# Performance work log

Measured on AMD Instinct MI355X. Metric: run time of the kernel, lower is better.

## Reference

```python
import jax, jax.numpy as jnp
import numpy as np

DT = 0.01
V_REST = 0.0


def setup_inputs() -> dict:
    key = jax.random.key(0)
    ks = jax.random.split(key, 9)
    S, N, T = 64, 128, 1000
    w = jax.random.normal(ks[0], (N, N), dtype=jnp.float32) / jnp.sqrt(jnp.float32(N))
    ic = jax.random.uniform(ks[1], (N,), dtype=jnp.float32)
    v0 = jax.random.uniform(ks[2], (S, N), dtype=jnp.float32)
    i0 = jax.random.uniform(ks[3], (S, N), dtype=jnp.float32)
    # spike-clock state starts at minus an Exponential(1) draw; event fires when it hits 0
    u0 = jax.random.uniform(ks[4], (S, N), dtype=jnp.float32, minval=1e-6, maxval=1.0)
    s0 = jnp.log(u0)
    mu = jax.random.uniform(ks[5], (2,), dtype=jnp.float32, minval=0.5, maxval=1.0)
    sg = jax.random.normal(ks[6], (2, 2), dtype=jnp.float32)
    sigma = 0.1 * jnp.dot(sg, sg.T)  # PSD diffusion matrix as in __init__
    noise = jax.random.normal(ks[7], (T, S, N, 2), dtype=jnp.float32)
    ue = jax.random.uniform(ks[8], (T, S, N), dtype=jnp.float32, minval=1e-6, maxval=1.0)
    exp_draws = -jnp.log(ue)
    return {"w": w, "ic": ic, "v0": v0, "i0": i0, "s0": s0,
            "mu": mu, "sigma": sigma, "noise": noise, "exp_draws": exp_draws}


def reference(w, ic, v0, i0, s0, mu, sigma, noise, exp_draws):
    """Euler-Maruyama integration of the spiking-neuron jump-SDE.

    Per neuron state y = (v, i, s):
      dv = mu1*(i + ic - v) dt + (sigma dW)_0
      di = -mu2*i dt        + (sigma dW)_1
      ds = intensity_fn(v) dt   (intensity_fn = softplus)
    Spike event when s crosses 0 (cond_fn = y[:, 2]):
      v -> v_rest, postsynaptic currents i += spikes @ w, s -> -Exp(1) redraw.
    Returns ys of shape (samples, neurons, times, 3).
    """
    mu1, mu2 = mu[0], mu[1]
    dW = noise * jnp.sqrt(jnp.asarray(DT, noise.dtype))  # [T,S,N,2]

    def step(carry, xs):
        v, i, s = carry
        dw, edraw = xs
        # drift
        dv = mu1 * (i + ic - v)
        di = -mu2 * i
        ds = jax.nn.softplus(v)  # intensity_fn
        # diffusion on (v,i) channels: sigma @ dW per neuron
        nvi = jnp.einsum('snk,jk->snj', dw, sigma)  # [S,N,2]
        v = v + DT * dv + nvi[..., 0]
        i = i + DT * di + nvi[..., 1]
        s = s + DT * ds
        spike = s >= 0.0  # event detection (cond_fn hits zero)
        spk = spike.astype(v.dtype)
        i = i + spk @ w                    # network coupling jump
        v = jnp.where(spike, V_REST, v)    # membrane reset
        s = jnp.where(spike, -edraw, s)    # redraw exponential spike clock
        return (v, i, s), jnp.stack([v, i, s], axis=-1)  # [S,N,3]

    (_, _, _), ys = jax.lax.scan(step, (v0, i0, s0), (dW, exp_draws))
    # ys: [T,S,N,3] -> [S,N,T,3] (samples, neurons, times, 3)
    return jnp.transpose(ys, (1, 2, 0, 3))
```

## Files before the change

kernel.cpp:

```cpp
#include <hip/hip_runtime.h>
#include <cmath>

#define NS 64
#define NN 128
#define NT 1000
#define CH 8
#define NNP 129
#define WROWS 130
#define WL_DW (WROWS * NN)
#define OB_HALF (CH * 3 * NNP)
#define OBUF_DW (2 * OB_HALF)
#define LDS_BYTES ((WL_DW + OBUF_DW) * 4 + 32)

__device__ __forceinline__ float softplus_np(float x) {
    float r = fmaxf(x, 0.0f) + log1pf(expf(-fabsf(x)));
    return (x == 0.0f) ? 0.693147180559945309f : r;
}

__device__ __forceinline__ void sync_lds() {
    __builtin_amdgcn_sched_barrier(0);
    asm volatile("s_waitcnt lgkmcnt(0)" ::: "memory");
    __builtin_amdgcn_s_barrier();
    __builtin_amdgcn_sched_barrier(0);
}

__global__ __launch_bounds__(192) void snn_scan_kernel(
    const float* __restrict__ w,
    const float* __restrict__ ic,
    const float* __restrict__ v0,
    const float* __restrict__ i0,
    const float* __restrict__ s0,
    const float* __restrict__ mu,
    const float* __restrict__ sigma,
    const float* __restrict__ noise,
    const float* __restrict__ exp_draws,
    float* __restrict__ out)
{
    #pragma clang fp contract(off)
    extern __shared__ float smem[];
    float* wl   = smem;
    float* obuf = smem + WL_DW;
    unsigned long long* mslot =
        (unsigned long long*)(smem + WL_DW + OBUF_DW);

    const int samp = blockIdx.x;
    const int tid  = threadIdx.x;
    const int wid  = tid >> 6;
    const int l    = tid & 63;
    const int n    = (wid << 6) | l;

    if (tid < 128) {
        const float4* src = (const float4*)w;
        float4* dst = (float4*)wl;
        #pragma unroll
        for (int it = 0; it < 32; ++it)
            dst[it * 128 + tid] = src[it * 128 + tid];
        ((float2*)(wl + NN * NN))[tid] = make_float2(0.0f, 0.0f);
    }

    const float SQDT  = sqrtf(0.01f);
    const float DTf   = 0.01f;
    const float LOGE2 = 0.693147180559945309f;

    float* outb = out + (size_t)samp * NN * NT * 3;

    float mu1 = 0.f, negmu2 = 0.f, g00 = 0.f, g01 = 0.f, g10 = 0.f, g11 = 0.f;
    float icn = 0.f, v_ = 0.f, i_ = 0.f, s_ = 0.f, sp = 0.f;
    float2 nb0 = {}, nb1 = {}, nb2 = {}, nb3 = {}, nb4 = {}, nb5 = {}, nb6 = {}, nb7 = {};
    float  eb0 = 0, eb1 = 0, eb2 = 0, eb3 = 0, eb4 = 0, eb5 = 0, eb6 = 0, eb7 = 0;

    const float* nzb = noise + (size_t)samp * (NN * 2) + n * 2;
    const float* edb = exp_draws + (size_t)samp * NN + n;

    if (wid < 2) {
        __builtin_amdgcn_s_setprio(1);
        mu1 = mu[0]; negmu2 = -mu[1];
        g00 = sigma[0]; g01 = sigma[1]; g10 = sigma[2]; g11 = sigma[3];
        icn = ic[n];
        v_ = v0[samp * NN + n];
        i_ = i0[samp * NN + n];
        s_ = s0[samp * NN + n];
        sp = softplus_np(v_);
        nb0 = *(const float2*)(nzb + 0ull * (NS * NN * 2)); eb0 = edb[0ull * (NS * NN)];
        nb1 = *(const float2*)(nzb + 1ull * (NS * NN * 2)); eb1 = edb[1ull * (NS * NN)];
        nb2 = *(const float2*)(nzb + 2ull * (NS * NN * 2)); eb2 = edb[2ull * (NS * NN)];
        nb3 = *(const float2*)(nzb + 3ull * (NS * NN * 2)); eb3 = edb[3ull * (NS * NN)];
        nb4 = *(const float2*)(nzb + 4ull * (NS * NN * 2)); eb4 = edb[4ull * (NS * NN)];
        nb5 = *(const float2*)(nzb + 5ull * (NS * NN * 2)); eb5 = edb[5ull * (NS * NN)];
        nb6 = *(const float2*)(nzb + 6ull * (NS * NN * 2)); eb6 = edb[6ull * (NS * NN)];
        nb7 = *(const float2*)(nzb + 7ull * (NS * NN * 2)); eb7 = edb[7ull * (NS * NN)];
    }
    sync_lds();

    if (wid < 2) {
        auto STEP = [&](int k, int blk, float2& nb, float& eb) {
            #pragma clang fp contract(off)
            const int t = blk * CH + k;
            s_ = s_ + DTf * sp;
            const bool kk = (s_ >= 0.0f);
            const unsigned long long mym = __ballot(kk);
            if (l == 0) mslot[(k & 1) * 2 + wid] = mym;
            sync_lds();
            const float2 nz = nb;
            const float  ed = eb;
            const int tp = (t + 8) < NT ? (t + 8) : NT - 1;
            nb = *(const float2*)(nzb + (size_t)tp * (NS * NN * 2));
            eb = edb[(size_t)tp * (NS * NN)];

            const float dw0 = nz.x * SQDT, dw1 = nz.y * SQDT;
            const float nv = (dw0 * g00) + (dw1 * g01);
            const float ni = (dw0 * g10) + (dw1 * g11);
            const float tt = (i_ + icn) - v_;
            const float vt = (v_ + DTf * (mu1 * tt)) + nv;
            const float it = (i_ + DTf * (negmu2 * i_)) + ni;
            const float spv = softplus_np(vt);

            unsigned long long m0 = mslot[(k & 1) * 2 + 0];
            unsigned long long m1 = mslot[(k & 1) * 2 + 1];

            float a = 0.0f;
            if (m0 | m1) {
                auto ext1 = [&]() -> int {
                    const bool u0 = (m0 != 0);
                    const unsigned long long m = u0 ? m0 : m1;
                    const int b = m ? (int)__builtin_ctzll(m) : 99;
                    const int r = (b == 99) ? 128 : ((u0 ? 0 : 64) + b);
                    const unsigned long long m0n = m0 & (m0 - 1);
                    const unsigned long long m1n = m1 & (m1 - 1);
                    m0 = u0 ? m0n : m0;
                    m1 = u0 ? m1 : m1n;
                    return r;
                };
                const int r1 = ext1(); const int r2 = ext1();
                const int r3 = ext1(); const int r4 = ext1();
                const float q1 = wl[r1 * NN + n];
                const float q2 = wl[r2 * NN + n];
                const float q3 = wl[r3 * NN + n];
                const float q4 = wl[r4 * NN + n];
                a = q1;  a += q2;  a += q3;  a += q4;
                #pragma clang loop unroll(disable)
                while (m0 | m1) {
                    const int r = ext1();
                    a += wl[r * NN + n];
                }
            }
            i_ = it + a;

            v_ = kk ? 0.0f : vt;
            s_ = kk ? -ed : s_;
            sp = kk ? LOGE2 : spv;

            float* row = obuf + (blk & 1) * OB_HALF + (k * 3) * NNP + n;
            row[0 * NNP] = v_;
            row[1 * NNP] = i_;
            row[2 * NNP] = s_;
        };

        #pragma clang loop unroll(disable)
        for (int blk = 0; blk < NT / CH; ++blk) {
            STEP(0, blk, nb0, eb0);
            STEP(1, blk, nb1, eb1);
            STEP(2, blk, nb2, eb2);
            STEP(3, blk, nb3, eb3);
            STEP(4, blk, nb4, eb4);
            STEP(5, blk, nb5, eb5);
            STEP(6, blk, nb6, eb6);
            STEP(7, blk, nb7, eb7);
        }
    } else {
        auto flush3 = [&](int h, int tb0, int kk) {
            const float* ob2 = obuf + h * OB_HALF;
            #pragma unroll
            for (int j = 3 * kk; j < 3 * kk + 3; ++j) {
                const int f = j * 64 + l;
                const int nn2 = f / 12;
                const int da = 2 * (f - nn2 * 12);
                const float x = ob2[(da    ) * NNP + nn2];
                const float y = ob2[(da + 1) * NNP + nn2];
                *(float2*)(outb + (size_t)nn2 * (NT * 3) + (size_t)tb0 * 3 + da) =
                    make_float2(x, y);
            }
        };
        #pragma clang loop unroll(disable)
        for (int blk = 0; blk < NT / CH; ++blk) {
            #pragma clang loop unroll(disable)
            for (int k = 0; k < CH; ++k) {
                sync_lds();
                if (blk > 0) flush3((blk - 1) & 1, (blk - 1) * CH, k);
            }
        }
    }

    sync_lds();
    if (wid == 2) {
        const float* ob2 = obuf + ((NT / CH - 1) & 1) * OB_HALF;
        #pragma unroll
        for (int j = 0; j < 24; ++j) {
            const int f = j * 64 + l;
            const int nn2 = f / 12;
            const int da = 2 * (f - nn2 * 12);
            const float x = ob2[(da    ) * NNP + nn2];
            const float y = ob2[(da + 1) * NNP + nn2];
            *(float2*)(outb + (size_t)nn2 * (NT * 3) + (size_t)(NT - CH) * 3 + da) =
                make_float2(x, y);
        }
    }
}

extern "C" void kernel_launch(void* const* d_in, const int* in_sizes, int n_in,
                              void* d_out, int out_size, void* d_ws, size_t ws_size,
                              hipStream_t stream) {
    const float* w         = (const float*)d_in[0];
    const float* ic        = (const float*)d_in[1];
    const float* v0        = (const float*)d_in[2];
    const float* i0        = (const float*)d_in[3];
    const float* s0        = (const float*)d_in[4];
    const float* mu        = (const float*)d_in[5];
    const float* sigma     = (const float*)d_in[6];
    const float* noise     = (const float*)d_in[7];
    const float* exp_draws = (const float*)d_in[8];
    float* out = (float*)d_out;

    (void)hipFuncSetAttribute((const void*)snn_scan_kernel,
                              hipFuncAttributeMaxDynamicSharedMemorySize,
                              LDS_BYTES);

    snn_scan_kernel<<<dim3(NS), dim3(192), LDS_BYTES, stream>>>(
        w, ic, v0, i0, s0, mu, sigma, noise, exp_draws, out);
}
```

Before: 569.7 us.

## Drop dedicated writer wave; store outputs directly from registers as float4

Removes the third wavefront that drained an LDS staging buffer to global memory, along with that buffer. Each compute thread now keeps its 8 timesteps × 3 values in registers and writes them as six float4 stores into its own contiguous output row. This cuts LDS traffic, barrier participants and block size, but the global stores now sit on the critical scan path and are strided across threads (each lane writes a different 12 KB row), so coalescing is poor.

```diff
diff --git a/kernel.cpp b/kernel.cpp
--- a/kernel.cpp
+++ b/kernel.cpp
@@ -5,12 +5,9 @@
 #define NN 128
 #define NT 1000
 #define CH 8
-#define NNP 129
 #define WROWS 130
 #define WL_DW (WROWS * NN)
-#define OB_HALF (CH * 3 * NNP)
-#define OBUF_DW (2 * OB_HALF)
-#define LDS_BYTES ((WL_DW + OBUF_DW) * 4 + 32)
+#define LDS_BYTES (WL_DW * 4 + 32)
 
 __device__ __forceinline__ float softplus_np(float x) {
     float r = fmaxf(x, 0.0f) + log1pf(expf(-fabsf(x)));
@@ -24,7 +21,7 @@
     __builtin_amdgcn_sched_barrier(0);
 }
 
-__global__ __launch_bounds__(192) void snn_scan_kernel(
+__global__ __launch_bounds__(128) void snn_scan_kernel(
     const float* __restrict__ w,
     const float* __restrict__ ic,
     const float* __restrict__ v0,
@@ -38,10 +35,9 @@
 {
     #pragma clang fp contract(off)
     extern __shared__ float smem[];
-    float* wl   = smem;
-    float* obuf = smem + WL_DW;
+    float* wl = smem;
     unsigned long long* mslot =
-        (unsigned long long*)(smem + WL_DW + OBUF_DW);
+        (unsigned long long*)(smem + WL_DW);
 
     const int samp = blockIdx.x;
     const int tid  = threadIdx.x;
@@ -49,7 +45,7 @@
     const int l    = tid & 63;
     const int n    = (wid << 6) | l;
 
-    if (tid < 128) {
+    {
         const float4* src = (const float4*)w;
         float4* dst = (float4*)wl;
         #pragma unroll
@@ -62,149 +58,113 @@
     const float DTf   = 0.01f;
     const float LOGE2 = 0.693147180559945309f;
 
-    float* outb = out + (size_t)samp * NN * NT * 3;
+    float* outb = out + ((size_t)samp * NN + n) * (NT * 3);
 
-    float mu1 = 0.f, negmu2 = 0.f, g00 = 0.f, g01 = 0.f, g10 = 0.f, g11 = 0.f;
-    float icn = 0.f, v_ = 0.f, i_ = 0.f, s_ = 0.f, sp = 0.f;
-    float2 nb0 = {}, nb1 = {}, nb2 = {}, nb3 = {}, nb4 = {}, nb5 = {}, nb6 = {}, nb7 = {};
-    float  eb0 = 0, eb1 = 0, eb2 = 0, eb3 = 0, eb4 = 0, eb5 = 0, eb6 = 0, eb7 = 0;
+    float mu1, negmu2, g00, g01, g10, g11, icn;
+    float v_, i_, s_, sp;
+    float2 nb0, nb1, nb2, nb3, nb4, nb5, nb6, nb7;
+    float  eb0, eb1, eb2, eb3, eb4, eb5, eb6, eb7;
 
     const float* nzb = noise + (size_t)samp * (NN * 2) + n * 2;
     const float* edb = exp_draws + (size_t)samp * NN + n;
 
-    if (wid < 2) {
-        __builtin_amdgcn_s_setprio(1);
-        mu1 = mu[0]; negmu2 = -mu[1];
-        g00 = sigma[0]; g01 = sigma[1]; g10 = sigma[2]; g11 = sigma[3];
-        icn = ic[n];
-        v_ = v0[samp * NN + n];
-        i_ = i0[samp * NN + n];
-        s_ = s0[samp * NN + n];
-        sp = softplus_np(v_);
-        nb0 = *(const float2*)(nzb + 0ull * (NS * NN * 2)); eb0 = edb[0ull * (NS * NN)];
-        nb1 = *(const float2*)(nzb + 1ull * (NS * NN * 2)); eb1 = edb[1ull * (NS * NN)];
-        nb2 = *(const float2*)(nzb + 2ull * (NS * NN * 2)); eb2 = edb[2ull * (NS * NN)];
-        nb3 = *(const float2*)(nzb + 3ull * (NS * NN * 2)); eb3 = edb[3ull * (NS * NN)];
-        nb4 = *(const float2*)(nzb + 4ull * (NS * NN * 2)); eb4 = edb[4ull * (NS * NN)];
-        nb5 = *(const float2*)(nzb + 5ull * (NS * NN * 2)); eb5 = edb[5ull * (NS * NN)];
-        nb6 = *(const float2*)(nzb + 6ull * (NS * NN * 2)); eb6 = edb[6ull * (NS * NN)];
-        nb7 = *(const float2*)(nzb + 7ull * (NS * NN * 2)); eb7 = edb[7ull * (NS * NN)];
-    }
+    mu1 = mu[0]; negmu2 = -mu[1];
+    g00 = sigma[0]; g01 = sigma[1]; g10 = sigma[2]; g11 = sigma[3];
+    icn = ic[n];
+    v_ = v0[samp * NN + n];
+    i_ = i0[samp * NN + n];
+    s_ = s0[samp * NN + n];
+    sp = softplus_np(v_);
+    nb0 = *(const float2*)(nzb + 0ull * (NS * NN * 2)); eb0 = edb[0ull * (NS * NN)];
+    nb1 = *(const float2*)(nzb + 1ull * (NS * NN * 2)); eb1 = edb[1ull * (NS * NN)];
+    nb2 = *(const float2*)(nzb + 2ull * (NS * NN * 2)); eb2 = edb[2ull * (NS * NN)];
+    nb3 = *(const float2*)(nzb + 3ull * (NS * NN * 2)); eb3 = edb[3ull * (NS * NN)];
+    nb4 = *(const float2*)(nzb + 4ull * (NS * NN * 2)); eb4 = edb[4ull * (NS * NN)];
+    nb5 = *(const float2*)(nzb + 5ull * (NS * NN * 2)); eb5 = edb[5ull * (NS * NN)];
+    nb6 = *(const float2*)(nzb + 6ull * (NS * NN * 2)); eb6 = edb[6ull * (NS * NN)];
+    nb7 = *(const float2*)(nzb + 7ull * (NS * NN * 2)); eb7 = edb[7ull * (NS * NN)];
+
     sync_lds();
 
-    if (wid < 2) {
-        auto STEP = [&](int k, int blk, float2& nb, float& eb) {
-            #pragma clang fp contract(off)
-            const int t = blk * CH + k;
-            s_ = s_ + DTf * sp;
-            const bool kk = (s_ >= 0.0f);
-            const unsigned long long mym = __ballot(kk);
-            if (l == 0) mslot[(k & 1) * 2 + wid] = mym;
-            sync_lds();
-            const float2 nz = nb;
-            const float  ed = eb;
-            const int tp = (t + 8) < NT ? (t + 8) : NT - 1;
-            nb = *(const float2*)(nzb + (size_t)tp * (NS * NN * 2));
-            eb = edb[(size_t)tp * (NS * NN)];
+    float o0, o1, o2, o3, o4, o5, o6, o7, o8, o9, o10, o11,
+          o12, o13, o14, o15, o16, o17, o18, o19, o20, o21, o22, o23;
 
-            const float dw0 = nz.x * SQDT, dw1 = nz.y * SQDT;
-            const float nv = (dw0 * g00) + (dw1 * g01);
-            const float ni = (dw0 * g10) + (dw1 * g11);
-            const float tt = (i_ + icn) - v_;
-            const float vt = (v_ + DTf * (mu1 * tt)) + nv;
-            const float it = (i_ + DTf * (negmu2 * i_)) + ni;
-            const float spv = softplus_np(vt);
-
-            unsigned long long m0 = mslot[(k & 1) * 2 + 0];
-            unsigned long long m1 = mslot[(k & 1) * 2 + 1];
-
-            float a = 0.0f;
-            if (m0 | m1) {
-                auto ext1 = [&]() -> int {
-                    const bool u0 = (m0 != 0);
-                    const unsigned long long m = u0 ? m0 : m1;
-                    const int b = m ? (int)__builtin_ctzll(m) : 99;
-                    const int r = (b == 99) ? 128 : ((u0 ? 0 : 64) + b);
-                    const unsigned long long m0n = m0 & (m0 - 1);
-                    const unsigned long long m1n = m1 & (m1 - 1);
-                    m0 = u0 ? m0n : m0;
-                    m1 = u0 ? m1 : m1n;
-                    return r;
-                };
-                const int r1 = ext1(); const int r2 = ext1();
-                const int r3 = ext1(); const int r4 = ext1();
-                const float q1 = wl[r1 * NN + n];
-                const float q2 = wl[r2 * NN + n];
-                const float q3 = wl[r3 * NN + n];
-                const float q4 = wl[r4 * NN + n];
-                a = q1;  a += q2;  a += q3;  a += q4;
-                #pragma clang loop unroll(disable)
-                while (m0 | m1) {
-                    const int r = ext1();
-                    a += wl[r * NN + n];
-                }
-            }
-            i_ = it + a;
-
-            v_ = kk ? 0.0f : vt;
-            s_ = kk ? -ed : s_;
-            sp = kk ? LOGE2 : spv;
-
-            float* row = obuf + (blk & 1) * OB_HALF + (k * 3) * NNP + n;
-            row[0 * NNP] = v_;
-            row[1 * NNP] = i_;
-            row[2 * NNP] = s_;
-        };
-
-        #pragma clang loop unroll(disable)
-        for (int blk = 0; blk < NT / CH; ++blk) {
-            STEP(0, blk, nb0, eb0);
-            STEP(1, blk, nb1, eb1);
-            STEP(2, blk, nb2, eb2);
-            STEP(3, blk, nb3, eb3);
-            STEP(4, blk, nb4, eb4);
-            STEP(5, blk, nb5, eb5);
-            STEP(6, blk, nb6, eb6);
-            STEP(7, blk, nb7, eb7);
-        }
-    } else {
-        auto flush3 = [&](int h, int tb0, int kk) {
-            const float* ob2 = obuf + h * OB_HALF;
-            #pragma unroll
-            for (int j = 3 * kk; j < 3 * kk + 3; ++j) {
-                const int f = j * 64 + l;
-                const int nn2 = f / 12;
-                const int da = 2 * (f - nn2 * 12);
-                const float x = ob2[(da    ) * NNP + nn2];
-                const float y = ob2[(da + 1) * NNP + nn2];
-                *(float2*)(outb + (size_t)nn2 * (NT * 3) + (size_t)tb0 * 3 + da) =
-                    make_float2(x, y);
-            }
-        };
-        #pragma clang loop unroll(disable)
-        for (int blk = 0; blk < NT / CH; ++blk) {
-            #pragma clang loop unroll(disable)
-            for (int k = 0; k < CH; ++k) {
-                sync_lds();
-                if (blk > 0) flush3((blk - 1) & 1, (blk - 1) * CH, k);
-            }
-        }
+    #define STEP(K, NB, EB, OV, OI, OS)                                        \
+    {                                                                          \
+        const int t = blk * CH + (K);                                          \
+                                \
+        s_ = s_ + DTf * sp;                                                    \
+        const bool kk = (s_ >= 0.0f);                                          \
+        const unsigned long long mym = __ballot(kk);                           \
+        if (l == 0) mslot[((K) & 1) * 2 + wid] = mym;                          \
+        sync_lds();                                                            \
+                \
+        const float2 nz = NB;                                                  \
+        const float  ed = EB;                                                  \
+        const int tp = (t + 8) < NT ? (t + 8) : NT - 1;                        \
+        NB = *(const float2*)(nzb + (size_t)tp * (NS * NN * 2));               \
+        EB = edb[(size_t)tp * (NS * NN)];                                      \
+        const float dw0 = nz.x * SQDT, dw1 = nz.y * SQDT;                      \
+        const float nv = (dw0 * g00) + (dw1 * g01);                            \
+        const float ni = (dw0 * g10) + (dw1 * g11);                            \
+        const float tt = (i_ + icn) - v_;                                      \
+        const float vt = (v_ + DTf * (mu1 * tt)) + nv;                         \
+        const float it = (i_ + DTf * (negmu2 * i_)) + ni;                      \
+        const float spv = softplus_np(vt);                                     \
+        unsigned long long m0 = mslot[((K) & 1) * 2 + 0];                      \
+        unsigned long long m1 = mslot[((K) & 1) * 2 + 1];                      \
+        float a = 0.0f;                                                        \
+        if (m0 | m1) {                                                         \
+            auto ext1 = [&]() -> int {                                         \
+                const bool u0 = (m0 != 0);                                     \
+                const unsigned long long m = u0 ? m0 : m1;                     \
+                const int b = m ? (int)__builtin_ctzll(m) : 99;                \
+                const int r = (b == 99) ? 128 : ((u0 ? 0 : 64) + b);           \
+                const unsigned long long m0n = m0 & (m0 - 1);                  \
+                const unsigned long long m1n = m1 & (m1 - 1);                  \
+                m0 = u0 ? m0n : m0;                                            \
+                m1 = u0 ? m1 : m1n;                                            \
+                return r;                                                      \
+            };                                                                 \
+            const int r1 = ext1(); const int r2 = ext1();                      \
+            const int r3 = ext1(); const int r4 = ext1();                      \
+            const float q1 = wl[r1 * NN + n];                                  \
+            const float q2 = wl[r2 * NN + n];                                  \
+            const float q3 = wl[r3 * NN + n];                                  \
+            const float q4 = wl[r4 * NN + n];                                  \
+            a = q1;  a += q2;  a += q3;  a += q4;                              \
+            _Pragma("clang loop unroll(disable)")                              \
+            while (m0 | m1) {                                                  \
+                const int r = ext1();                                          \
+                a += wl[r * NN + n];                                           \
+            }                                                                  \
+        }                                                                      \
+        i_ = it + a;                                                           \
+        v_ = kk ? 0.0f : vt;                                                   \
+        s_ = kk ? -ed : s_;                                                    \
+        sp = kk ? LOGE2 : spv;                                                 \
+        OV = v_; OI = i_; OS = s_;                                             \
     }
 
-    sync_lds();
-    if (wid == 2) {
-        const float* ob2 = obuf + ((NT / CH - 1) & 1) * OB_HALF;
-        #pragma unroll
-        for (int j = 0; j < 24; ++j) {
-            const int f = j * 64 + l;
-            const int nn2 = f / 12;
-            const int da = 2 * (f - nn2 * 12);
-            const float x = ob2[(da    ) * NNP + nn2];
-            const float y = ob2[(da + 1) * NNP + nn2];
-            *(float2*)(outb + (size_t)nn2 * (NT * 3) + (size_t)(NT - CH) * 3 + da) =
-                make_float2(x, y);
-        }
+    #pragma clang loop unroll(disable)
+    for (int blk = 0; blk < NT / CH; ++blk) {
+        STEP(0, nb0, eb0, o0,  o1,  o2 );
+        STEP(1, nb1, eb1, o3,  o4,  o5 );
+        STEP(2, nb2, eb2, o6,  o7,  o8 );
+        STEP(3, nb3, eb3, o9,  o10, o11);
+        STEP(4, nb4, eb4, o12, o13, o14);
+        STEP(5, nb5, eb5, o15, o16, o17);
+        STEP(6, nb6, eb6, o18, o19, o20);
+        STEP(7, nb7, eb7, o21, o22, o23);
+        float* ob = outb + blk * (CH * 3);
+        *(float4*)(ob +  0) = make_float4(o0,  o1,  o2,  o3 );
+        *(float4*)(ob +  4) = make_float4(o4,  o5,  o6,  o7 );
+        *(float4*)(ob +  8) = make_float4(o8,  o9,  o10, o11);
+        *(float4*)(ob + 12) = make_float4(o12, o13, o14, o15);
+        *(float4*)(ob + 16) = make_float4(o16, o17, o18, o19);
+        *(float4*)(ob + 20) = make_float4(o20, o21, o22, o23);
     }
+    #undef STEP
 }
 
 extern "C" void kernel_launch(void* const* d_in, const int* in_sizes, int n_in,
@@ -225,6 +185,6 @@
                               hipFuncAttributeMaxDynamicSharedMemorySize,
                               LDS_BYTES);
 
-    snn_scan_kernel<<<dim3(NS), dim3(192), LDS_BYTES, stream>>>(
+    snn_scan_kernel<<<dim3(NS), dim3(128), LDS_BYTES, stream>>>(
         w, ic, v0, i0, s0, mu, sigma, noise, exp_draws, out);
 }
```

New measurement: 584.7 us. 2.6% more time.

## Defer spike-coupling accumulation to next step to shorten the serial critical path

Applied to the files above, without the earlier changes.

The sum of coupling weights gathered from spike masks is no longer added into the current right after the barrier. It is finished in the next step, before that step's barrier, and the completed current is written to the output buffer one step late. The v, s and softplus updates now no longer wait on the LDS gather. The flush warp shifts to writing four chunks in slots 1-6 to match the delayed i writes. This adds bookkeeping state and care at the wrap-around and final-step edges.

```diff
diff --git a/kernel.cpp b/kernel.cpp
--- a/kernel.cpp
+++ b/kernel.cpp
@@ -65,7 +65,11 @@
     float* outb = out + (size_t)samp * NN * NT * 3;
 
     float mu1 = 0.f, negmu2 = 0.f, g00 = 0.f, g01 = 0.f, g10 = 0.f, g11 = 0.f;
-    float icn = 0.f, v_ = 0.f, i_ = 0.f, s_ = 0.f, sp = 0.f;
+    float icn = 0.f, v_ = 0.f, s_ = 0.f, sp = 0.f;
+    float it_prev = 0.f;
+    float q1v = 0.f, q2v = 0.f, q3v = 0.f, q4v = 0.f;
+    float afull = 0.f;
+    bool  fullf = true;
     float2 nb0 = {}, nb1 = {}, nb2 = {}, nb3 = {}, nb4 = {}, nb5 = {}, nb6 = {}, nb7 = {};
     float  eb0 = 0, eb1 = 0, eb2 = 0, eb3 = 0, eb4 = 0, eb5 = 0, eb6 = 0, eb7 = 0;
 
@@ -78,9 +82,10 @@
         g00 = sigma[0]; g01 = sigma[1]; g10 = sigma[2]; g11 = sigma[3];
         icn = ic[n];
         v_ = v0[samp * NN + n];
-        i_ = i0[samp * NN + n];
+        it_prev = i0[samp * NN + n];
         s_ = s0[samp * NN + n];
         sp = softplus_np(v_);
+        afull = 0.0f; fullf = true;
         nb0 = *(const float2*)(nzb + 0ull * (NS * NN * 2)); eb0 = edb[0ull * (NS * NN)];
         nb1 = *(const float2*)(nzb + 1ull * (NS * NN * 2)); eb1 = edb[1ull * (NS * NN)];
         nb2 = *(const float2*)(nzb + 2ull * (NS * NN * 2)); eb2 = edb[2ull * (NS * NN)];
@@ -100,6 +105,14 @@
             const bool kk = (s_ >= 0.0f);
             const unsigned long long mym = __ballot(kk);
             if (l == 0) mslot[(k & 1) * 2 + wid] = mym;
+            float a;
+            if (fullf) a = afull;
+            else { a = q1v; a += q2v; a += q3v; a += q4v; }
+            const float i_cur = it_prev + a;
+            {
+                const int tm1 = (t == 0) ? 15 : (t - 1);
+                obuf[((tm1 >> 3) & 1) * OB_HALF + ((tm1 & 7) * 3 + 1) * NNP + n] = i_cur;
+            }
             sync_lds();
             const float2 nz = nb;
             const float  ed = eb;
@@ -110,15 +123,24 @@
             const float dw0 = nz.x * SQDT, dw1 = nz.y * SQDT;
             const float nv = (dw0 * g00) + (dw1 * g01);
             const float ni = (dw0 * g10) + (dw1 * g11);
-            const float tt = (i_ + icn) - v_;
+            const float tt = (i_cur + icn) - v_;
             const float vt = (v_ + DTf * (mu1 * tt)) + nv;
-            const float it = (i_ + DTf * (negmu2 * i_)) + ni;
+            const float it = (i_cur + DTf * (negmu2 * i_cur)) + ni;
             const float spv = softplus_np(vt);
 
             unsigned long long m0 = mslot[(k & 1) * 2 + 0];
             unsigned long long m1 = mslot[(k & 1) * 2 + 1];
 
-            float a = 0.0f;
+            v_ = kk ? 0.0f : vt;
+            s_ = kk ? -ed : s_;
+            sp = kk ? LOGE2 : spv;
+
+            {
+                float* row = obuf + (blk & 1) * OB_HALF + (k * 3) * NNP + n;
+                row[0 * NNP] = v_;
+                row[2 * NNP] = s_;
+            }
+
             if (m0 | m1) {
                 auto ext1 = [&]() -> int {
                     const bool u0 = (m0 != 0);
@@ -133,27 +155,25 @@
                 };
                 const int r1 = ext1(); const int r2 = ext1();
                 const int r3 = ext1(); const int r4 = ext1();
-                const float q1 = wl[r1 * NN + n];
-                const float q2 = wl[r2 * NN + n];
-                const float q3 = wl[r3 * NN + n];
-                const float q4 = wl[r4 * NN + n];
-                a = q1;  a += q2;  a += q3;  a += q4;
-                #pragma clang loop unroll(disable)
-                while (m0 | m1) {
-                    const int r = ext1();
-                    a += wl[r * NN + n];
+                q1v = wl[r1 * NN + n];
+                q2v = wl[r2 * NN + n];
+                q3v = wl[r3 * NN + n];
+                q4v = wl[r4 * NN + n];
+                if (m0 | m1) {
+                    float a2 = q1v; a2 += q2v; a2 += q3v; a2 += q4v;
+                    #pragma clang loop unroll(disable)
+                    do {
+                        const int r = ext1();
+                        a2 += wl[r * NN + n];
+                    } while (m0 | m1);
+                    afull = a2; fullf = true;
+                } else {
+                    fullf = false;
                 }
-            }
-            i_ = it + a;
-
-            v_ = kk ? 0.0f : vt;
-            s_ = kk ? -ed : s_;
-            sp = kk ? LOGE2 : spv;
-
-            float* row = obuf + (blk & 1) * OB_HALF + (k * 3) * NNP + n;
-            row[0 * NNP] = v_;
-            row[1 * NNP] = i_;
-            row[2 * NNP] = s_;
+            } else {
+                afull = 0.0f; fullf = true;
+            }
+            it_prev = it;
         };
 
         #pragma clang loop unroll(disable)
@@ -167,11 +187,19 @@
             STEP(6, blk, nb6, eb6);
             STEP(7, blk, nb7, eb7);
         }
+
+        {
+            float a;
+            if (fullf) a = afull;
+            else { a = q1v; a += q2v; a += q3v; a += q4v; }
+            const float ifin = it_prev + a;
+            obuf[0 * OB_HALF + (7 * 3 + 1) * NNP + n] = ifin;
+        }
     } else {
-        auto flush3 = [&](int h, int tb0, int kk) {
+        auto flush4 = [&](int h, int tb0, int slot) {
             const float* ob2 = obuf + h * OB_HALF;
             #pragma unroll
-            for (int j = 3 * kk; j < 3 * kk + 3; ++j) {
+            for (int j = 4 * (slot - 1); j < 4 * slot; ++j) {
                 const int f = j * 64 + l;
                 const int nn2 = f / 12;
                 const int da = 2 * (f - nn2 * 12);
@@ -186,14 +214,15 @@
             #pragma clang loop unroll(disable)
             for (int k = 0; k < CH; ++k) {
                 sync_lds();
-                if (blk > 0) flush3((blk - 1) & 1, (blk - 1) * CH, k);
+                if (blk > 0 && k >= 1 && k <= 6)
+                    flush4((blk - 1) & 1, (blk - 1) * CH, k);
             }
         }
     }
 
     sync_lds();
     if (wid == 2) {
-        const float* ob2 = obuf + ((NT / CH - 1) & 1) * OB_HALF;
+        const float* ob2 = obuf + 0 * OB_HALF;
         #pragma unroll
         for (int j = 0; j < 24; ++j) {
             const int f = j * 64 + l;
```

New measurement: 599.9 us. 5.3% more time.
